# Performance work log

Measured on AMD Instinct MI355X. Metric: run time of the kernel, lower is better.

The kernel has to match this reference:

```python
import jax, jax.numpy as jnp
import numpy as np

N_STATES = 4097  # 4096 hidden + bookend state 0
N_OBVS = 4097    # 4096 symbols + bookend symbol 0
T = 2048         # observation sequence length


def setup_inputs() -> dict:
    key = jax.random.key(0)
    k1, k2, k3 = jax.random.split(key, 3)
    # log_pi: start in bookend state 0 with prob ~1.
    log_pi = jnp.full((N_STATES,), -99.0, dtype=jnp.float32).at[0].set(0.0)
    # Row-stochastic transition log-probs (matches log_softmax(dim=1) init).
    log_trans = jax.nn.log_softmax(
        jax.random.normal(k1, (N_STATES, N_STATES), dtype=jnp.float32), axis=1)
    log_trans = log_trans.at[0, 0].set(-99.0)
    # Categorical emission log-prob table [state, symbol].
    log_em = jax.nn.log_softmax(
        jax.random.normal(k2, (N_STATES, N_OBVS), dtype=jnp.float32), axis=1)
    # Observed symbols, never the bookend symbol 0.
    obvs = jax.random.randint(k3, (T,), 1, N_OBVS, dtype=jnp.int32)
    return {"log_pi": log_pi, "log_trans": log_trans, "log_em": log_em, "obvs": obvs}


def reference(log_pi, log_trans, log_em, obvs):
    """HMM.log_forward_scan: log evidence via the forward algorithm.

    Recurrence: log_fs <- emission(obs) + logsumexp_k(log_fs[k] + log_trans[k, :]).
    Termination: logsumexp(log_fs + log_trans[:, 0]) (return to bookend state).
    """
    def step(log_fs, obs):
        # [S, 1] + [S, S] -> logsumexp over source states -> [S]
        new_fs = log_em[:, obs] + jax.nn.logsumexp(log_fs[:, None] + log_trans, axis=0)
        return new_fs, None

    log_fs, _ = jax.lax.scan(step, log_pi, obvs)
    return jax.nn.logsumexp(log_fs + log_trans[:, 0])
```

## Files before the change

kernel.cpp:

```cpp
#include <hip/hip_runtime.h>

#define S       4097
#define KP      4160
#define NBLK    256
#define NTHR    1024
#define PSTRIDE 4104

typedef int   i32x4  __attribute__((ext_vector_type(4)));
typedef float f32x4  __attribute__((ext_vector_type(4)));
typedef short bf16x8 __attribute__((ext_vector_type(8)));

__device__ __forceinline__ float blo(unsigned int u) { return __uint_as_float(u << 16); }
__device__ __forceinline__ float bhi(unsigned int u) { return __uint_as_float(u & 0xffff0000u); }
__device__ __forceinline__ unsigned short rne_bf16(float x) {
  unsigned u = __float_as_uint(x);
  return (unsigned short)((u + 0x7fffu + ((u >> 16) & 1u)) >> 16);
}

__global__ void __launch_bounds__(NTHR) hmm_persist(
    const float* __restrict__ log_pi, const float* __restrict__ log_trans,
    const float* __restrict__ log_em, const int* __restrict__ obvs,
    int* __restrict__ packs, float* __restrict__ basep, int T)
{
  __shared__ __align__(16) unsigned short plds[17 * KP];
  __shared__ __align__(16) unsigned short vb[KP];
  __shared__ __align__(16) float part[8][256];
  __shared__ float red[16];
  __shared__ float em_lds[17];
  __shared__ float part2[8];

  const int tid = threadIdx.x, lane = tid & 63, wid = tid >> 6;
  const int b = blockIdx.x, jb = b * 16;
  const int ncols = (b == NBLK - 1) ? 17 : 16;

  for (int idx = tid; idx < ncols * KP; idx += NTHR) {
    int k = idx / ncols, r = idx - k * ncols;
    float p = (k < S) ? __expf(log_trans[(size_t)k * S + (jb + r)]) : 0.f;
    plds[r * KP + ((((k >> 3) ^ (r & 7)) << 3) | (k & 7))] = rne_bf16(p);
  }
  if (tid < KP - S) vb[S + tid] = 0;
  float Bacc = 0.f;
  float s    = 0.f;
  __syncthreads();

  const int   kb0 = (wid & 7) * 16;
  const int   rr  = lane & 15, r7 = rr & 7;
  const int   g   = lane >> 4;
  const uint4* ap = ((const uint4*)plds) + rr * (KP / 8);
  const uint4* vp = (const uint4*)vb;
  bf16x8 pre[8];
  #pragma unroll
  for (int i = 0; i < 8; ++i)
    pre[i] = __builtin_bit_cast(bf16x8, ap[((kb0 + i) * 4 + g) ^ r7]);

  for (int t = 0; t < T; ++t) {
    const int* pin  = packs + ((t + 1) & 1) * PSTRIDE;
    int*       pout = packs + (t & 1) * PSTRIDE;
    const int  obs  = obvs[t];

    if (t > 0) {
      float mn = red[lane & 15];
      #pragma unroll
      for (int off = 8; off; off >>= 1) mn = fmaxf(mn, __shfl_xor(mn, off, 64));
      s = mn;
    }
    Bacc += s;

    float emv = 0.f;
    if (wid == 15 && lane < ncols) emv = log_em[(size_t)(jb + lane) * S + obs];

    float va0, va1, va2, va3, va4 = -3.4e38f;
    if (t == 0) {
      const float4 v4 = *(const float4*)(log_pi + 4 * tid);
      va0 = v4.x; va1 = v4.y; va2 = v4.z; va3 = v4.w;
      if (tid == 0) va4 = log_pi[4096];
    } else {
      const int* pa = pin + 4 * tid;
      const int* pe = pin + 4096;
      i32x4 A; int E = 0;
      for (;;) {
        asm volatile("global_load_dwordx4 %0, %1, off sc0 sc1"
                     : "=&v"(A) : "v"(pa) : "memory");
        if (tid == 0)
          asm volatile("global_load_dword %0, %1, off sc0 sc1"
                       : "=&v"(E) : "v"(pe) : "memory");
        asm volatile("s_waitcnt vmcnt(0)" ::: "memory");
        __builtin_amdgcn_sched_barrier(0);
        bool ok = ((A.x & 0xffff) >= t) & ((A.y & 0xffff) >= t) &
                  ((A.z & 0xffff) >= t) & ((A.w & 0xffff) >= t);
        if (tid == 0) ok &= ((E & 0xffff) >= t);
        if (ok) {
          va0 = bhi(A.x); va1 = bhi(A.y); va2 = bhi(A.z); va3 = bhi(A.w);
          if (tid == 0) va4 = bhi(E);
          break;
        }
        __builtin_amdgcn_s_sleep(1);
      }
    }

    float v0 = __expf(va0 - s), v1 = __expf(va1 - s);
    float v2 = __expf(va2 - s), v3 = __expf(va3 - s);
    unsigned b0 = rne_bf16(v0), b1 = rne_bf16(v1);
    unsigned b2 = rne_bf16(v2), b3 = rne_bf16(v3);
    *(int2*)(vb + 4 * tid) = make_int2((int)((b1 << 16) | b0), (int)((b3 << 16) | b2));
    if (tid == 0)
      *(int*)(vb + 4096) = (int)rne_bf16(__expf(va4 - s));
    if (wid == 15 && lane < ncols) em_lds[lane] = emv;

    float rmx = fmaxf(fmaxf(va0, va1), fmaxf(fmaxf(va2, va3), va4));
    #pragma unroll
    for (int off = 32; off; off >>= 1) rmx = fmaxf(rmx, __shfl_xor(rmx, off, 64));
    if (lane == 0) red[wid] = rmx;
    __syncthreads();

    if (wid < 8) {
      const int kbn = (wid == 7) ? 17 : 16;
      f32x4 accA = {0.f, 0.f, 0.f, 0.f}, accB = {0.f, 0.f, 0.f, 0.f};
      #pragma unroll
      for (int i = 0; i < 8; i += 2) {
        bf16x8 w0 = __builtin_bit_cast(bf16x8, vp[(kb0 + i) * 4 + g]);
        accA = __builtin_amdgcn_mfma_f32_16x16x32_bf16(pre[i], w0, accA, 0, 0, 0);
        bf16x8 w1 = __builtin_bit_cast(bf16x8, vp[(kb0 + i + 1) * 4 + g]);
        accB = __builtin_amdgcn_mfma_f32_16x16x32_bf16(pre[i + 1], w1, accB, 0, 0, 0);
      }
      for (int mm = kb0 + 8; mm + 1 < kb0 + kbn; mm += 2) {
        bf16x8 a0 = __builtin_bit_cast(bf16x8, ap[(mm * 4 + g) ^ r7]);
        bf16x8 w0 = __builtin_bit_cast(bf16x8, vp[mm * 4 + g]);
        accA = __builtin_amdgcn_mfma_f32_16x16x32_bf16(a0, w0, accA, 0, 0, 0);
        bf16x8 a1 = __builtin_bit_cast(bf16x8, ap[((mm + 1) * 4 + g) ^ r7]);
        bf16x8 w1 = __builtin_bit_cast(bf16x8, vp[(mm + 1) * 4 + g]);
        accB = __builtin_amdgcn_mfma_f32_16x16x32_bf16(a1, w1, accB, 0, 0, 0);
      }
      if (kbn & 1) {
        int mm = kb0 + kbn - 1;
        bf16x8 a0 = __builtin_bit_cast(bf16x8, ap[(mm * 4 + g) ^ r7]);
        bf16x8 w0 = __builtin_bit_cast(bf16x8, vp[mm * 4 + g]);
        accA = __builtin_amdgcn_mfma_f32_16x16x32_bf16(a0, w0, accA, 0, 0, 0);
      }
      accA += accB;
      *(f32x4*)&part[wid][lane * 4] = accA;
    } else if (b == NBLK - 1) {
      float a16 = 0.f;
      const uint4* prow = (const uint4*)(plds + 16 * KP);
      for (int ot = (wid - 8) * 64 + lane; ot < KP / 8; ot += 512) {
        uint4 pw = prow[ot], vw = vp[ot];
        a16 += blo(pw.x) * blo(vw.x) + bhi(pw.x) * bhi(vw.x);
        a16 += blo(pw.y) * blo(vw.y) + bhi(pw.y) * bhi(vw.y);
        a16 += blo(pw.z) * blo(vw.z) + bhi(pw.z) * bhi(vw.z);
        a16 += blo(pw.w) * blo(vw.w) + bhi(pw.w) * bhi(vw.w);
      }
      #pragma unroll
      for (int off = 32; off; off >>= 1) a16 += __shfl_xor(a16, off, 64);
      if (lane == 0) part2[wid - 8] = a16;
    }
    __syncthreads();

    const int tag = t + 1;
    if (wid == 15) {
      f32x4 tot = {0.f, 0.f, 0.f, 0.f};
      #pragma unroll
      for (int p = 0; p < 8; ++p) tot += *(const f32x4*)&part[p][lane * 4];
      if ((lane & 15) == 0) {
        const int j0 = (lane >> 4) * 4;
        float d0 = em_lds[j0 + 0] + __logf(tot.x);
        float d1 = em_lds[j0 + 1] + __logf(tot.y);
        float d2 = em_lds[j0 + 2] + __logf(tot.z);
        float d3 = em_lds[j0 + 3] + __logf(tot.w);
        i32x4 o;
        o.x = ((int)rne_bf16(d0) << 16) | tag;
        o.y = ((int)rne_bf16(d1) << 16) | tag;
        o.z = ((int)rne_bf16(d2) << 16) | tag;
        o.w = ((int)rne_bf16(d3) << 16) | tag;
        const int* dst = pout + jb + j0;
        asm volatile("global_store_dwordx4 %0, %1, off sc0 sc1"
                     :: "v"(dst), "v"(o) : "memory");
      }
      if (b == NBLK - 1 && lane == 0) {
        float s16 = 0.f;
        #pragma unroll
        for (int p = 0; p < 8; ++p) s16 += part2[p];
        float d16 = em_lds[16] + __logf(s16);
        int o16 = ((int)rne_bf16(d16) << 16) | tag;
        const int* dst = pout + 4096;
        asm volatile("global_store_dword %0, %1, off sc0 sc1"
                     :: "v"(dst), "v"(o16) : "memory");
      }
    }
    __syncthreads();
  }
  if (b == 0 && tid == 0) basep[0] = Bacc;
}

__global__ void __launch_bounds__(1024) hmm_final(
    const int* __restrict__ dq, const float* __restrict__ log_trans,
    const float* __restrict__ basep, float* __restrict__ out)
{
  __shared__ float red[16];
  const int tid = threadIdx.x, lane = tid & 63, wid = tid >> 6;
  float va[5];
  float rmax = -3.4e38f;
  #pragma unroll
  for (int i = 0; i < 5; ++i) {
    int k = tid + i * 1024;
    va[i] = (k < S) ? (bhi(dq[k]) + log_trans[(size_t)k * S]) : -3.4e38f;
    rmax = fmaxf(rmax, va[i]);
  }
  #pragma unroll
  for (int off = 32; off; off >>= 1) rmax = fmaxf(rmax, __shfl_xor(rmax, off, 64));
  if (lane == 0) red[wid] = rmax;
  __syncthreads();
  float m = red[0];
  #pragma unroll
  for (int i = 1; i < 16; ++i) m = fmaxf(m, red[i]);
  float s = 0.f;
  #pragma unroll
  for (int i = 0; i < 5; ++i) s += __expf(va[i] - m);
  #pragma unroll
  for (int off = 32; off; off >>= 1) s += __shfl_xor(s, off, 64);
  __syncthreads();
  if (lane == 0) red[wid] = s;
  __syncthreads();
  if (tid == 0) {
    float tot = 0.f;
    #pragma unroll
    for (int i = 0; i < 16; ++i) tot += red[i];
    out[0] = basep[0] + m + __logf(tot);
  }
}

extern "C" void kernel_launch(void* const* d_in, const int* in_sizes, int n_in,
                              void* d_out, int out_size, void* d_ws, size_t ws_size,
                              hipStream_t stream) {
  const float* log_pi    = (const float*)d_in[0];
  const float* log_trans = (const float*)d_in[1];
  const float* log_em    = (const float*)d_in[2];
  const int*   obvs      = (const int*)d_in[3];
  const int    T         = in_sizes[3];

  int*   packs = (int*)d_ws;
  float* basep = (float*)((char*)d_ws + 2 * PSTRIDE * 4);

  hipMemsetAsync(packs, 0, 2 * PSTRIDE * 4, stream);
  hipLaunchKernelGGL(hmm_persist, dim3(NBLK), dim3(NTHR), 0, stream,
                     log_pi, log_trans, log_em, obvs, packs, basep, T);
  const int* fsT = packs + (size_t)((T - 1) & 1) * PSTRIDE;
  hipLaunchKernelGGL(hmm_final, dim3(1), dim3(1024), 0, stream,
                     fsT, log_trans, basep, (float*)d_out);
}
```

Before: 5.685 ms.

## Cache all A fragments in registers, drop a per-step barrier, use hardware bf16 pack

Preloads all 17 transition-matrix MFMA fragments into registers, so the per-step loop no longer reads them from LDS. Removes the trailing __syncthreads in each time step by placing the barrier before the write to the max-reduction scratch. Replaces the manual bf16 rounding with the v_cvt_pk_bf16_f32 instruction when packing the state vector and the outputs. The larger register footprint with 1024 threads per block risks spills, and the barrier reordering relies on careful LDS reuse ordering across steps.

New measurement: 7.080 ms. 24.5% more time.

```diff
diff --git a/kernel.cpp b/kernel.cpp
--- a/kernel.cpp
+++ b/kernel.cpp
@@ -15,6 +15,11 @@
 __device__ __forceinline__ unsigned short rne_bf16(float x) {
   unsigned u = __float_as_uint(x);
   return (unsigned short)((u + 0x7fffu + ((u >> 16) & 1u)) >> 16);
+}
+__device__ __forceinline__ unsigned pk_bf16(float a, float b) {
+  unsigned r;
+  asm("v_cvt_pk_bf16_f32 %0, %1, %2" : "=v"(r) : "v"(a), "v"(b));
+  return r;
 }
 
 __global__ void __launch_bounds__(NTHR) hmm_persist(
@@ -48,9 +53,9 @@
   const int   g   = lane >> 4;
   const uint4* ap = ((const uint4*)plds) + rr * (KP / 8);
   const uint4* vp = (const uint4*)vb;
-  bf16x8 pre[8];
-  #pragma unroll
-  for (int i = 0; i < 8; ++i)
+  bf16x8 pre[17];
+  #pragma unroll
+  for (int i = 0; i < 17; ++i)
     pre[i] = __builtin_bit_cast(bf16x8, ap[((kb0 + i) * 4 + g) ^ r7]);
 
   for (int t = 0; t < T; ++t) {
@@ -100,9 +105,7 @@
 
     float v0 = __expf(va0 - s), v1 = __expf(va1 - s);
     float v2 = __expf(va2 - s), v3 = __expf(va3 - s);
-    unsigned b0 = rne_bf16(v0), b1 = rne_bf16(v1);
-    unsigned b2 = rne_bf16(v2), b3 = rne_bf16(v3);
-    *(int2*)(vb + 4 * tid) = make_int2((int)((b1 << 16) | b0), (int)((b3 << 16) | b2));
+    *(int2*)(vb + 4 * tid) = make_int2((int)pk_bf16(v0, v1), (int)pk_bf16(v2, v3));
     if (tid == 0)
       *(int*)(vb + 4096) = (int)rne_bf16(__expf(va4 - s));
     if (wid == 15 && lane < ncols) em_lds[lane] = emv;
@@ -110,32 +113,19 @@
     float rmx = fmaxf(fmaxf(va0, va1), fmaxf(fmaxf(va2, va3), va4));
     #pragma unroll
     for (int off = 32; off; off >>= 1) rmx = fmaxf(rmx, __shfl_xor(rmx, off, 64));
+    __syncthreads();
     if (lane == 0) red[wid] = rmx;
-    __syncthreads();
 
     if (wid < 8) {
       const int kbn = (wid == 7) ? 17 : 16;
       f32x4 accA = {0.f, 0.f, 0.f, 0.f}, accB = {0.f, 0.f, 0.f, 0.f};
       #pragma unroll
-      for (int i = 0; i < 8; i += 2) {
-        bf16x8 w0 = __builtin_bit_cast(bf16x8, vp[(kb0 + i) * 4 + g]);
-        accA = __builtin_amdgcn_mfma_f32_16x16x32_bf16(pre[i], w0, accA, 0, 0, 0);
-        bf16x8 w1 = __builtin_bit_cast(bf16x8, vp[(kb0 + i + 1) * 4 + g]);
-        accB = __builtin_amdgcn_mfma_f32_16x16x32_bf16(pre[i + 1], w1, accB, 0, 0, 0);
-      }
-      for (int mm = kb0 + 8; mm + 1 < kb0 + kbn; mm += 2) {
-        bf16x8 a0 = __builtin_bit_cast(bf16x8, ap[(mm * 4 + g) ^ r7]);
-        bf16x8 w0 = __builtin_bit_cast(bf16x8, vp[mm * 4 + g]);
-        accA = __builtin_amdgcn_mfma_f32_16x16x32_bf16(a0, w0, accA, 0, 0, 0);
-        bf16x8 a1 = __builtin_bit_cast(bf16x8, ap[((mm + 1) * 4 + g) ^ r7]);
-        bf16x8 w1 = __builtin_bit_cast(bf16x8, vp[(mm + 1) * 4 + g]);
-        accB = __builtin_amdgcn_mfma_f32_16x16x32_bf16(a1, w1, accB, 0, 0, 0);
-      }
-      if (kbn & 1) {
-        int mm = kb0 + kbn - 1;
-        bf16x8 a0 = __builtin_bit_cast(bf16x8, ap[(mm * 4 + g) ^ r7]);
-        bf16x8 w0 = __builtin_bit_cast(bf16x8, vp[mm * 4 + g]);
-        accA = __builtin_amdgcn_mfma_f32_16x16x32_bf16(a0, w0, accA, 0, 0, 0);
+      for (int i = 0; i < 17; ++i) {
+        if (i < kbn) {
+          bf16x8 w = __builtin_bit_cast(bf16x8, vp[(kb0 + i) * 4 + g]);
+          if (i & 1) accB = __builtin_amdgcn_mfma_f32_16x16x32_bf16(pre[i], w, accB, 0, 0, 0);
+          else       accA = __builtin_amdgcn_mfma_f32_16x16x32_bf16(pre[i], w, accA, 0, 0, 0);
+        }
       }
       accA += accB;
       *(f32x4*)&part[wid][lane * 4] = accA;
@@ -166,11 +156,12 @@
         float d1 = em_lds[j0 + 1] + __logf(tot.y);
         float d2 = em_lds[j0 + 2] + __logf(tot.z);
         float d3 = em_lds[j0 + 3] + __logf(tot.w);
+        unsigned u01 = pk_bf16(d0, d1), u23 = pk_bf16(d2, d3);
         i32x4 o;
-        o.x = ((int)rne_bf16(d0) << 16) | tag;
-        o.y = ((int)rne_bf16(d1) << 16) | tag;
-        o.z = ((int)rne_bf16(d2) << 16) | tag;
-        o.w = ((int)rne_bf16(d3) << 16) | tag;
+        o.x = (int)((u01 << 16) | (unsigned)tag);
+        o.y = (int)((u01 & 0xffff0000u) | (unsigned)tag);
+        o.z = (int)((u23 << 16) | (unsigned)tag);
+        o.w = (int)((u23 & 0xffff0000u) | (unsigned)tag);
         const int* dst = pout + jb + j0;
         asm volatile("global_store_dwordx4 %0, %1, off sc0 sc1"
                      :: "v"(dst), "v"(o) : "memory");
@@ -180,13 +171,12 @@
         #pragma unroll
         for (int p = 0; p < 8; ++p) s16 += part2[p];
         float d16 = em_lds[16] + __logf(s16);
-        int o16 = ((int)rne_bf16(d16) << 16) | tag;
+        int o16 = (int)(((unsigned)rne_bf16(d16) << 16) | (unsigned)tag);
         const int* dst = pout + 4096;
         asm volatile("global_store_dword %0, %1, off sc0 sc1"
                      :: "v"(dst), "v"(o16) : "memory");
       }
     }
-    __syncthreads();
   }
   if (b == 0 && tid == 0) basep[0] = Bacc;
 }
@@ -240,7 +230,7 @@
   int*   packs = (int*)d_ws;
   float* basep = (float*)((char*)d_ws + 2 * PSTRIDE * 4);
 
-  hipMemsetAsync(packs, 0, 2 * PSTRIDE * 4, stream);
+  (void)hipMemsetAsync(packs, 0, 2 * PSTRIDE * 4, stream);
   hipLaunchKernelGGL(hmm_persist, dim3(NBLK), dim3(NTHR), 0, stream,
                      log_pi, log_trans, log_em, obvs, packs, basep, T);
   const int* fsT = packs + (size_t)((T - 1) & 1) * PSTRIDE;
```
